# Optimization experiments

Hardware: AMD Instinct MI355X
Metric: run time of the kernel (lower is better)

The kernel has to match this reference:

```python
import jax, jax.numpy as jnp
import numpy as np

D, NH, NKV, HD, FFN = 2560, 8, 4, 256, 10240
QD = NH * HD
CTX = 4096
EPS = 1e-6


def _rms(x, eps=EPS):
    # Equivalent to F.layer_norm(cat([x,-x]), 2D): zero mean, var = mean(x^2)
    return x * jax.lax.rsqrt(jnp.mean(jnp.square(x), axis=-1, keepdims=True) + eps)


def rmsnorm(x, w):
    # Gemma-style ANERMSNorm with learnable scale (1 + w)
    return _rms(x) * (1.0 + w)


def rotate_half(x):
    x1, x2 = jnp.split(x, 2, axis=-1)
    return jnp.concatenate([-x2, x1], axis=-1)


def setup_inputs() -> dict:
    key = jax.random.key(0)
    ks = jax.random.split(key, 16)
    s = 0.02
    return {
        "x": jax.random.normal(ks[0], (1, 1, D), jnp.float32),
        "cos": jax.random.uniform(ks[1], (1, 1, HD), jnp.float32, -1.0, 1.0),
        "sin": jax.random.uniform(ks[2], (1, 1, HD), jnp.float32, -1.0, 1.0),
        "mask": jnp.zeros((1, 1, 1, CTX), jnp.float32),
        "cache_k": jax.random.normal(ks[3], (1, NKV, CTX, HD), jnp.float32),
        "cache_v": jax.random.normal(ks[4], (1, NKV, CTX, HD), jnp.float32),
        "ctx_len": CTX,
        "w_in_ln": jax.random.normal(ks[5], (D,), jnp.float32) * s,
        "w_post_attn_ln": jax.random.normal(ks[6], (D,), jnp.float32) * s,
        "w_pre_ffn_ln": jax.random.normal(ks[7], (D,), jnp.float32) * s,
        "w_post_ffn_ln": jax.random.normal(ks[8], (D,), jnp.float32) * s,
        "Wq": jax.random.normal(ks[9], (QD, D), jnp.float32) * s,
        "Wo": jax.random.normal(ks[10], (D, QD), jnp.float32) * s,
        "Wg": jax.random.normal(ks[11], (FFN, D), jnp.float32) * s,
        "Wu": jax.random.normal(ks[12], (FFN, D), jnp.float32) * s,
        "Wd": jax.random.normal(ks[13], (D, FFN), jnp.float32) * s,
    }


def reference(x, cos, sin, mask, cache_k, cache_v, ctx_len,
              w_in_ln, w_post_attn_ln, w_pre_ffn_ln, w_post_ffn_ln,
              Wq, Wo, Wg, Wu, Wd):
    rep = NH // NKV
    residual = x
    h = rmsnorm(x, w_in_ln)                      # (1,1,D)
    q = h @ Wq.T                                 # (1,1,QD)  1x1-conv == linear
    q = q.reshape(1, 1, NH, HD)
    q = _rms(q)                                  # q_norm, no learnable weight
    q = q.transpose(0, 2, 1, 3)                  # (1,NH,1,HD)
    q = q * cos[:, None] + rotate_half(q) * sin[:, None]
    k = jnp.repeat(cache_k, rep, axis=1)         # (1,NH,L,HD) GQA expand
    v = jnp.repeat(cache_v, rep, axis=1)
    scores = jnp.einsum("bhqd,bhkd->bhqk", q, k) * 1.0 + mask
    attn = jax.nn.softmax(scores, axis=-1)       # numerically stable softmax
    a = jnp.einsum("bhqk,bhkd->bhqd", attn, v)   # (1,NH,1,HD)
    a = a.transpose(0, 2, 1, 3).reshape(1, 1, QD)
    a = a @ Wo.T                                 # (1,1,D)
    x = residual + rmsnorm(a, w_post_attn_ln)
    residual = x
    h = rmsnorm(x, w_pre_ffn_ln)
    g = jax.nn.gelu(h @ Wg.T, approximate=True)  # tanh-approx GELU
    ffn = (g * (h @ Wu.T)) @ Wd.T                # GeGLU down-proj
    x = residual + rmsnorm(ffn, w_post_ffn_ln)
    return x
```

## Files before the change

### kernel.cpp

```cpp
#include <hip/hip_runtime.h>

#define D_    2560
#define NH_   8
#define NKV_  4
#define HD_   256
#define FFN_  10240
#define QD_   2048
#define CTX_  4096
#define EPSF  1e-6f
#define SCH   128
#define WCH   64

typedef float f4 __attribute__((ext_vector_type(4)));

__device__ __forceinline__ float wave_red_sum(float v) {
#pragma unroll
    for (int o = 32; o > 0; o >>= 1) v += __shfl_down(v, o, 64);
    return v;
}

__device__ __forceinline__ float block_red_sum(float v) {
    __shared__ float s[4];
    __shared__ float tot;
    int lane = threadIdx.x & 63, w = threadIdx.x >> 6;
    v = wave_red_sum(v);
    if (lane == 0) s[w] = v;
    __syncthreads();
    if (threadIdx.x == 0) tot = s[0] + s[1] + s[2] + s[3];
    __syncthreads();
    return tot;
}

__device__ __forceinline__ float block_red_max(float v) {
    __shared__ float s[4];
    __shared__ float tot;
    int lane = threadIdx.x & 63, w = threadIdx.x >> 6;
#pragma unroll
    for (int o = 32; o > 0; o >>= 1) v = fmaxf(v, __shfl_down(v, o, 64));
    if (lane == 0) s[w] = v;
    __syncthreads();
    if (threadIdx.x == 0) tot = fmaxf(fmaxf(s[0], s[1]), fmaxf(s[2], s[3]));
    __syncthreads();
    return tot;
}

template <int COLS>
__global__ __launch_bounds__(256) void k_gemv_nt(const float* __restrict__ W,
                                                 const float* __restrict__ x,
                                                 float* __restrict__ y) {
    constexpr int NC = COLS / 4;
    constexpr int CPL = NC / 64;
    __shared__ f4 xs[NC];
    int t = threadIdx.x;
    for (int i = t; i < NC; i += 256) xs[i] = ((const f4*)x)[i];
    __syncthreads();
    int lane = t & 63;
    int row = blockIdx.x * 4 + (t >> 6);
    const f4* Wr = (const f4*)W + (size_t)row * NC + lane;
    f4 wv[CPL];
#pragma unroll
    for (int k = 0; k < CPL; k++) wv[k] = __builtin_nontemporal_load(Wr + k * 64);
    float acc = 0.f;
#pragma unroll
    for (int k = 0; k < CPL; k++) {
        f4 xx = xs[lane + k * 64];
        acc += wv[k].x * xx.x + wv[k].y * xx.y + wv[k].z * xx.z + wv[k].w * xx.w;
    }
    acc = wave_red_sum(acc);
    if (lane == 0) y[row] = acc;
}

__global__ __launch_bounds__(256) void k_geglu_nt(const float* __restrict__ Wg,
                                                  const float* __restrict__ Wu,
                                                  const float* __restrict__ h,
                                                  float* __restrict__ gu) {
    __shared__ f4 xs[640];
    int t = threadIdx.x;
    for (int i = t; i < 640; i += 256) xs[i] = ((const f4*)h)[i];
    __syncthreads();
    int lane = t & 63;
    int row = blockIdx.x * 4 + (t >> 6);
    const f4* G = (const f4*)Wg + (size_t)row * 640 + lane;
    const f4* U = (const f4*)Wu + (size_t)row * 640 + lane;
    f4 wg[10], wu[10];
#pragma unroll
    for (int k = 0; k < 10; k++) wg[k] = __builtin_nontemporal_load(G + k * 64);
#pragma unroll
    for (int k = 0; k < 10; k++) wu[k] = __builtin_nontemporal_load(U + k * 64);
    float ag = 0.f, au = 0.f;
#pragma unroll
    for (int k = 0; k < 10; k++) {
        f4 xx = xs[lane + k * 64];
        ag += wg[k].x * xx.x + wg[k].y * xx.y + wg[k].z * xx.z + wg[k].w * xx.w;
        au += wu[k].x * xx.x + wu[k].y * xx.y + wu[k].z * xx.z + wu[k].w * xx.w;
    }
#pragma unroll
    for (int o = 32; o > 0; o >>= 1) {
        ag += __shfl_down(ag, o, 64);
        au += __shfl_down(au, o, 64);
    }
    if (lane == 0) {
        float g = ag;
        float tt = tanhf(0.7978845608028654f * (g + 0.044715f * g * g * g));
        gu[row] = 0.5f * g * (1.f + tt) * au;
    }
}

__global__ __launch_bounds__(256) void k_wd_nt(const float* __restrict__ Wd,
                                               const float* __restrict__ gu,
                                               float* __restrict__ ffn) {
    __shared__ f4 xs[2560];
    int t = threadIdx.x;
    for (int i = t; i < 2560; i += 256) xs[i] = ((const f4*)gu)[i];
    __syncthreads();
    int lane = t & 63;
    int row = blockIdx.x * 4 + (t >> 6);
    const f4* Wr = (const f4*)Wd + (size_t)row * 2560 + lane;
    float acc = 0.f;
#pragma unroll
    for (int g = 0; g < 4; g++) {
        f4 wv[10];
#pragma unroll
        for (int k = 0; k < 10; k++)
            wv[k] = __builtin_nontemporal_load(Wr + (g * 10 + k) * 64);
#pragma unroll
        for (int k = 0; k < 10; k++) {
            f4 xx = xs[lane + (g * 10 + k) * 64];
            acc += wv[k].x * xx.x + wv[k].y * xx.y + wv[k].z * xx.z + wv[k].w * xx.w;
        }
    }
    acc = wave_red_sum(acc);
    if (lane == 0) ffn[row] = acc;
}

__global__ void k_res_rms(const float* __restrict__ res,
                          const float* __restrict__ a,
                          const float* __restrict__ w1, float* __restrict__ out1,
                          const float* __restrict__ w2, float* __restrict__ out2) {
    const int K = D_ / 256;
    int t = threadIdx.x;
    float va[K];
    float ss = 0.f;
#pragma unroll
    for (int k = 0; k < K; k++) {
        int i = t + k * 256;
        va[k] = a[i];
        ss += va[k] * va[k];
    }
    float tot = block_red_sum(ss);
    float rs = rsqrtf(tot / (float)D_ + EPSF);
    float vo[K];
    float ss2 = 0.f;
#pragma unroll
    for (int k = 0; k < K; k++) {
        int i = t + k * 256;
        float r = res ? res[i] : 0.f;
        vo[k] = r + va[k] * rs * (1.f + w1[i]);
        out1[i] = vo[k];
        ss2 += vo[k] * vo[k];
    }
    if (out2) {
        float tot2 = block_red_sum(ss2);
        float rs2 = rsqrtf(tot2 / (float)D_ + EPSF);
#pragma unroll
        for (int k = 0; k < K; k++) {
            int i = t + k * 256;
            out2[i] = vo[k] * rs2 * (1.f + w2[i]);
        }
    }
}

__global__ void k_qnorm_rope(const float* __restrict__ qraw,
                             const float* __restrict__ cosv,
                             const float* __restrict__ sinv,
                             float* __restrict__ qout) {
    __shared__ float qn[HD_];
    int h = blockIdx.x, d = threadIdx.x;
    float v = qraw[h * HD_ + d];
    float tot = block_red_sum(v * v);
    float rs = rsqrtf(tot / (float)HD_ + EPSF);
    float n = v * rs;
    qn[d] = n;
    __syncthreads();
    float rot = (d < HD_ / 2) ? -qn[d + HD_ / 2] : qn[d - HD_ / 2];
    qout[h * HD_ + d] = n * cosv[d] + rot * sinv[d];
}

__global__ __launch_bounds__(256) void k_scores(const float* __restrict__ Kc,
                                                const float* __restrict__ q,
                                                const float* __restrict__ mask,
                                                float* __restrict__ s) {
    int kvh = blockIdx.x, chunk = blockIdx.y;
    int lane = threadIdx.x & 63, w = threadIdx.x >> 6;
    int h0 = 2 * kvh, h1 = h0 + 1;
    const f4* q4 = (const f4*)q;
    f4 q0 = q4[h0 * 64 + lane];
    f4 q1 = q4[h1 * 64 + lane];
    int lbase = chunk * (CTX_ / SCH) + w * 8;
    const f4* Kb = (const f4*)(Kc + ((size_t)kvh * CTX_ + lbase) * HD_) + lane;
    f4 kk[8];
#pragma unroll
    for (int i = 0; i < 8; i++) kk[i] = Kb[i * 64];
    float d0[8], d1[8];
#pragma unroll
    for (int i = 0; i < 8; i++) {
        d0[i] = kk[i].x * q0.x + kk[i].y * q0.y + kk[i].z * q0.z + kk[i].w * q0.w;
        d1[i] = kk[i].x * q1.x + kk[i].y * q1.y + kk[i].z * q1.z + kk[i].w * q1.w;
    }
#pragma unroll
    for (int o = 32; o > 0; o >>= 1) {
#pragma unroll
        for (int i = 0; i < 8; i++) {
            d0[i] += __shfl_down(d0[i], o, 64);
            d1[i] += __shfl_down(d1[i], o, 64);
        }
    }
    if (lane == 0) {
#pragma unroll
        for (int i = 0; i < 8; i++) {
            int l = lbase + i;
            float m = mask[l];
            s[(size_t)h0 * CTX_ + l] = d0[i] + m;
            s[(size_t)h1 * CTX_ + l] = d1[i] + m;
        }
    }
}

__global__ void k_softmax(float* __restrict__ s) {
    int h = blockIdx.x, t = threadIdx.x;
    float* sh = s + (size_t)h * CTX_;
    float m = -1e30f;
    for (int l = t; l < CTX_; l += 256) m = fmaxf(m, sh[l]);
    m = block_red_max(m);
    float sum = 0.f;
    for (int l = t; l < CTX_; l += 256) {
        float e = expf(sh[l] - m);
        sh[l] = e;
        sum += e;
    }
    sum = block_red_sum(sum);
    float inv = 1.f / sum;
    for (int l = t; l < CTX_; l += 256) sh[l] *= inv;
}

__global__ __launch_bounds__(256) void k_wv(const float* __restrict__ V,
                                            const float* __restrict__ p,
                                            float* __restrict__ part) {
    int kvh = blockIdx.x, chunk = blockIdx.y, d = threadIdx.x;
    int h0 = 2 * kvh, h1 = h0 + 1;
    constexpr int R = CTX_ / WCH;
    __shared__ float p0[R], p1[R];
    int l0 = chunk * R;
    if (d < R) p0[d] = p[(size_t)h0 * CTX_ + l0 + d];
    else if (d < 2 * R) p1[d - R] = p[(size_t)h1 * CTX_ + l0 + d - R];
    __syncthreads();
    const float* Vb = V + ((size_t)kvh * CTX_ + l0) * HD_;
    float a0 = 0.f, a1 = 0.f;
#pragma unroll 8
    for (int li = 0; li < R; li++) {
        float v = Vb[(size_t)li * HD_ + d];
        a0 += p0[li] * v;
        a1 += p1[li] * v;
    }
    part[((h0 * WCH) + chunk) * HD_ + d] = a0;
    part[((h1 * WCH) + chunk) * HD_ + d] = a1;
}

__global__ void k_reduce_a(const float* __restrict__ part, float* __restrict__ a) {
    int h = blockIdx.x, d = threadIdx.x;
    float s = 0.f;
#pragma unroll
    for (int c = 0; c < WCH; c++) s += part[((h * WCH) + c) * HD_ + d];
    a[h * HD_ + d] = s;
}

extern "C" void kernel_launch(void* const* d_in, const int* in_sizes, int n_in,
                              void* d_out, int out_size, void* d_ws, size_t ws_size,
                              hipStream_t stream) {
    const float* x     = (const float*)d_in[0];
    const float* cosv  = (const float*)d_in[1];
    const float* sinv  = (const float*)d_in[2];
    const float* mask  = (const float*)d_in[3];
    const float* cK    = (const float*)d_in[4];
    const float* cV    = (const float*)d_in[5];
    const float* w_in  = (const float*)d_in[7];
    const float* w_pa  = (const float*)d_in[8];
    const float* w_pf  = (const float*)d_in[9];
    const float* w_pff = (const float*)d_in[10];
    const float* Wq    = (const float*)d_in[11];
    const float* Wo    = (const float*)d_in[12];
    const float* Wg    = (const float*)d_in[13];
    const float* Wu    = (const float*)d_in[14];
    const float* Wd    = (const float*)d_in[15];

    float* ws   = (float*)d_ws;
    float* h    = ws;
    float* qraw = ws + 2560;
    float* q    = ws + 4608;
    float* sc   = ws + 6656;
    float* pwv  = ws + 39424;
    float* a    = ws + 170496;
    float* ao   = ws + 172544;
    float* x2   = ws + 175104;
    float* h2   = ws + 177664;
    float* gu   = ws + 180224;
    float* ffn  = ws + 190464;
    float* out  = (float*)d_out;

    k_res_rms<<<1, 256, 0, stream>>>(nullptr, x, w_in, h, nullptr, nullptr);
    k_gemv_nt<D_><<<QD_ / 4, 256, 0, stream>>>(Wq, h, qraw);
    k_qnorm_rope<<<NH_, HD_, 0, stream>>>(qraw, cosv, sinv, q);
    k_scores<<<dim3(NKV_, SCH), 256, 0, stream>>>(cK, q, mask, sc);
    k_softmax<<<NH_, 256, 0, stream>>>(sc);
    k_wv<<<dim3(NKV_, WCH), 256, 0, stream>>>(cV, sc, pwv);
    k_reduce_a<<<NH_, HD_, 0, stream>>>(pwv, a);
    k_gemv_nt<QD_><<<D_ / 4, 256, 0, stream>>>(Wo, a, ao);
    k_res_rms<<<1, 256, 0, stream>>>(x, ao, w_pa, x2, w_pf, h2);
    k_geglu_nt<<<FFN_ / 4, 256, 0, stream>>>(Wg, Wu, h2, gu);
    k_wd_nt<<<D_ / 4, 256, 0, stream>>>(Wd, gu, ffn);
    k_res_rms<<<1, 256, 0, stream>>>(x2, ffn, w_pff, out, nullptr, nullptr);
}
```

Baseline: 106.5 us.

## Use persistent grid-stride GEMV kernels and split Wd rows into four partial segments

Replaces the fixed one-row-per-wave GEMV kernels with persistent grid-stride kernels using fixed grids of 512 or 640 blocks. The input vector is now read straight from global memory instead of being staged in shared memory. The Wd down-projection is split into four 640-wide segments per output row, and the final residual-RMSNorm kernel sums the partials. The goal is more loads in flight per wave for Wd, plus lower block launch and shared-memory staging overhead. The cost is repeated global (cached) reads of the input vector and an extra partial-sum pass.

```diff
diff --git a/kernel.cpp b/kernel.cpp
--- a/kernel.cpp
+++ b/kernel.cpp
@@ -44,97 +44,93 @@
     return tot;
 }
 
-template <int COLS>
-__global__ __launch_bounds__(256) void k_gemv_nt(const float* __restrict__ W,
-                                                 const float* __restrict__ x,
-                                                 float* __restrict__ y) {
-    constexpr int NC = COLS / 4;
-    constexpr int CPL = NC / 64;
-    __shared__ f4 xs[NC];
-    int t = threadIdx.x;
-    for (int i = t; i < NC; i += 256) xs[i] = ((const f4*)x)[i];
-    __syncthreads();
-    int lane = t & 63;
-    int row = blockIdx.x * 4 + (t >> 6);
-    const f4* Wr = (const f4*)W + (size_t)row * NC + lane;
-    f4 wv[CPL];
-#pragma unroll
-    for (int k = 0; k < CPL; k++) wv[k] = __builtin_nontemporal_load(Wr + k * 64);
-    float acc = 0.f;
-#pragma unroll
-    for (int k = 0; k < CPL; k++) {
-        f4 xx = xs[lane + k * 64];
-        acc += wv[k].x * xx.x + wv[k].y * xx.y + wv[k].z * xx.z + wv[k].w * xx.w;
-    }
-    acc = wave_red_sum(acc);
-    if (lane == 0) y[row] = acc;
-}
-
-__global__ __launch_bounds__(256) void k_geglu_nt(const float* __restrict__ Wg,
-                                                  const float* __restrict__ Wu,
-                                                  const float* __restrict__ h,
-                                                  float* __restrict__ gu) {
-    __shared__ f4 xs[640];
-    int t = threadIdx.x;
-    for (int i = t; i < 640; i += 256) xs[i] = ((const f4*)h)[i];
-    __syncthreads();
-    int lane = t & 63;
-    int row = blockIdx.x * 4 + (t >> 6);
-    const f4* G = (const f4*)Wg + (size_t)row * 640 + lane;
-    const f4* U = (const f4*)Wu + (size_t)row * 640 + lane;
-    f4 wg[10], wu[10];
-#pragma unroll
-    for (int k = 0; k < 10; k++) wg[k] = __builtin_nontemporal_load(G + k * 64);
-#pragma unroll
-    for (int k = 0; k < 10; k++) wu[k] = __builtin_nontemporal_load(U + k * 64);
-    float ag = 0.f, au = 0.f;
-#pragma unroll
-    for (int k = 0; k < 10; k++) {
-        f4 xx = xs[lane + k * 64];
-        ag += wg[k].x * xx.x + wg[k].y * xx.y + wg[k].z * xx.z + wg[k].w * xx.w;
-        au += wu[k].x * xx.x + wu[k].y * xx.y + wu[k].z * xx.z + wu[k].w * xx.w;
-    }
-#pragma unroll
-    for (int o = 32; o > 0; o >>= 1) {
-        ag += __shfl_down(ag, o, 64);
-        au += __shfl_down(au, o, 64);
-    }
-    if (lane == 0) {
-        float g = ag;
-        float tt = tanhf(0.7978845608028654f * (g + 0.044715f * g * g * g));
-        gu[row] = 0.5f * g * (1.f + tt) * au;
-    }
-}
-
-__global__ __launch_bounds__(256) void k_wd_nt(const float* __restrict__ Wd,
-                                               const float* __restrict__ gu,
-                                               float* __restrict__ ffn) {
-    __shared__ f4 xs[2560];
-    int t = threadIdx.x;
-    for (int i = t; i < 2560; i += 256) xs[i] = ((const f4*)gu)[i];
-    __syncthreads();
-    int lane = t & 63;
-    int row = blockIdx.x * 4 + (t >> 6);
-    const f4* Wr = (const f4*)Wd + (size_t)row * 2560 + lane;
-    float acc = 0.f;
-#pragma unroll
-    for (int g = 0; g < 4; g++) {
+template <int CPL>
+__global__ __launch_bounds__(256) void k_gemv_p(const float* __restrict__ W,
+                                                const float* __restrict__ x,
+                                                float* __restrict__ y, int ntask) {
+    int lane = threadIdx.x & 63;
+    int gw = (blockIdx.x * 256 + threadIdx.x) >> 6;
+    int nw = (gridDim.x * 256) >> 6;
+    const f4* X = (const f4*)x;
+    for (int t = gw; t < ntask; t += nw) {
+        const f4* Wr = (const f4*)W + (size_t)t * (CPL * 64) + lane;
+        f4 wv[CPL];
+#pragma unroll
+        for (int k = 0; k < CPL; k++) wv[k] = __builtin_nontemporal_load(Wr + k * 64);
+        float acc = 0.f;
+#pragma unroll
+        for (int k = 0; k < CPL; k++) {
+            f4 xx = X[k * 64 + lane];
+            acc += wv[k].x * xx.x + wv[k].y * xx.y + wv[k].z * xx.z + wv[k].w * xx.w;
+        }
+        acc = wave_red_sum(acc);
+        if (lane == 0) y[t] = acc;
+    }
+}
+
+__global__ __launch_bounds__(256) void k_geglu_p(const float* __restrict__ Wg,
+                                                 const float* __restrict__ Wu,
+                                                 const float* __restrict__ h,
+                                                 float* __restrict__ gu) {
+    int lane = threadIdx.x & 63;
+    int gw = (blockIdx.x * 256 + threadIdx.x) >> 6;
+    int nw = (gridDim.x * 256) >> 6;
+    const f4* X = (const f4*)h;
+    for (int t = gw; t < FFN_; t += nw) {
+        const f4* G = (const f4*)Wg + (size_t)t * 640 + lane;
+        const f4* U = (const f4*)Wu + (size_t)t * 640 + lane;
+        f4 wg[10], wu[10];
+#pragma unroll
+        for (int k = 0; k < 10; k++) wg[k] = __builtin_nontemporal_load(G + k * 64);
+#pragma unroll
+        for (int k = 0; k < 10; k++) wu[k] = __builtin_nontemporal_load(U + k * 64);
+        float ag = 0.f, au = 0.f;
+#pragma unroll
+        for (int k = 0; k < 10; k++) {
+            f4 xx = X[k * 64 + lane];
+            ag += wg[k].x * xx.x + wg[k].y * xx.y + wg[k].z * xx.z + wg[k].w * xx.w;
+            au += wu[k].x * xx.x + wu[k].y * xx.y + wu[k].z * xx.z + wu[k].w * xx.w;
+        }
+#pragma unroll
+        for (int o = 32; o > 0; o >>= 1) {
+            ag += __shfl_down(ag, o, 64);
+            au += __shfl_down(au, o, 64);
+        }
+        if (lane == 0) {
+            float g = ag;
+            float tt = tanhf(0.7978845608028654f * (g + 0.044715f * g * g * g));
+            gu[t] = 0.5f * g * (1.f + tt) * au;
+        }
+    }
+}
+
+__global__ __launch_bounds__(256) void k_wd_p(const float* __restrict__ Wd,
+                                              const float* __restrict__ gu,
+                                              float* __restrict__ part) {
+    int lane = threadIdx.x & 63;
+    int gw = (blockIdx.x * 256 + threadIdx.x) >> 6;
+    int nw = (gridDim.x * 256) >> 6;
+    const f4* X = (const f4*)gu;
+    for (int t = gw; t < D_ * 4; t += nw) {
+        int seg = t & 3;
+        const f4* Wr = (const f4*)Wd + (size_t)t * 640 + lane;
         f4 wv[10];
 #pragma unroll
-        for (int k = 0; k < 10; k++)
-            wv[k] = __builtin_nontemporal_load(Wr + (g * 10 + k) * 64);
+        for (int k = 0; k < 10; k++) wv[k] = __builtin_nontemporal_load(Wr + k * 64);
+        const f4* xw = X + seg * 640 + lane;
+        float acc = 0.f;
 #pragma unroll
         for (int k = 0; k < 10; k++) {
-            f4 xx = xs[lane + (g * 10 + k) * 64];
+            f4 xx = xw[k * 64];
             acc += wv[k].x * xx.x + wv[k].y * xx.y + wv[k].z * xx.z + wv[k].w * xx.w;
         }
-    }
-    acc = wave_red_sum(acc);
-    if (lane == 0) ffn[row] = acc;
+        acc = wave_red_sum(acc);
+        if (lane == 0) part[t] = acc;
+    }
 }
 
 __global__ void k_res_rms(const float* __restrict__ res,
-                          const float* __restrict__ a,
+                          const float* __restrict__ apart, int slots,
                           const float* __restrict__ w1, float* __restrict__ out1,
                           const float* __restrict__ w2, float* __restrict__ out2) {
     const int K = D_ / 256;
@@ -144,8 +140,10 @@
 #pragma unroll
     for (int k = 0; k < K; k++) {
         int i = t + k * 256;
-        va[k] = a[i];
-        ss += va[k] * va[k];
+        float v = 0.f;
+        for (int s = 0; s < slots; s++) v += apart[(size_t)i * slots + s];
+        va[k] = v;
+        ss += v * v;
     }
     float tot = block_red_sum(ss);
     float rs = rsqrtf(tot / (float)D_ + EPSF);
@@ -293,30 +291,30 @@
     const float* Wu    = (const float*)d_in[14];
     const float* Wd    = (const float*)d_in[15];
 
-    float* ws   = (float*)d_ws;
-    float* h    = ws;
-    float* qraw = ws + 2560;
-    float* q    = ws + 4608;
-    float* sc   = ws + 6656;
-    float* pwv  = ws + 39424;
-    float* a    = ws + 170496;
-    float* ao   = ws + 172544;
-    float* x2   = ws + 175104;
-    float* h2   = ws + 177664;
-    float* gu   = ws + 180224;
-    float* ffn  = ws + 190464;
-    float* out  = (float*)d_out;
-
-    k_res_rms<<<1, 256, 0, stream>>>(nullptr, x, w_in, h, nullptr, nullptr);
-    k_gemv_nt<D_><<<QD_ / 4, 256, 0, stream>>>(Wq, h, qraw);
+    float* ws    = (float*)d_ws;
+    float* h     = ws;
+    float* qraw  = ws + 2560;
+    float* q     = ws + 4608;
+    float* sc    = ws + 6656;
+    float* pwv   = ws + 39424;
+    float* a     = ws + 170496;
+    float* ao    = ws + 172544;
+    float* x2    = ws + 175104;
+    float* h2    = ws + 177664;
+    float* gu    = ws + 180224;
+    float* partd = ws + 190464;
+    float* out   = (float*)d_out;
+
+    k_res_rms<<<1, 256, 0, stream>>>(nullptr, x, 1, w_in, h, nullptr, nullptr);
+    k_gemv_p<10><<<512, 256, 0, stream>>>(Wq, h, qraw, QD_);
     k_qnorm_rope<<<NH_, HD_, 0, stream>>>(qraw, cosv, sinv, q);
     k_scores<<<dim3(NKV_, SCH), 256, 0, stream>>>(cK, q, mask, sc);
     k_softmax<<<NH_, 256, 0, stream>>>(sc);
     k_wv<<<dim3(NKV_, WCH), 256, 0, stream>>>(cV, sc, pwv);
     k_reduce_a<<<NH_, HD_, 0, stream>>>(pwv, a);
-    k_gemv_nt<QD_><<<D_ / 4, 256, 0, stream>>>(Wo, a, ao);
-    k_res_rms<<<1, 256, 0, stream>>>(x, ao, w_pa, x2, w_pf, h2);
-    k_geglu_nt<<<FFN_ / 4, 256, 0, stream>>>(Wg, Wu, h2, gu);
-    k_wd_nt<<<D_ / 4, 256, 0, stream>>>(Wd, gu, ffn);
-    k_res_rms<<<1, 256, 0, stream>>>(x2, ffn, w_pff, out, nullptr, nullptr);
-}
+    k_gemv_p<8><<<640, 256, 0, stream>>>(Wo, a, ao, D_);
+    k_res_rms<<<1, 256, 0, stream>>>(x, ao, 1, w_pa, x2, w_pf, h2);
+    k_geglu_p<<<512, 256, 0, stream>>>(Wg, Wu, h2, gu);
+    k_wd_p<<<512, 256, 0, stream>>>(Wd, gu, partd);
+    k_res_rms<<<1, 256, 0, stream>>>(x2, partd, 4, w_pff, out, nullptr, nullptr);
+}
```

Result: slower. 114.6 us (+7.6%).
